# Optimization experiments

Measured on AMD Instinct MI355X. Metric: run time of the kernel, lower is better.

The kernel has to match this reference:

```python
import jax, jax.numpy as jnp
import numpy as np

D_MODEL = 1024
D_FF = 4096
EPS = 1e-6


def _rms_norm(x, eps=EPS):
    var = jnp.mean(x * x, axis=-1, keepdims=True) + eps
    return x * jax.lax.rsqrt(var)


def setup_inputs() -> dict:
    key = jax.random.key(0)
    kx, kw = jax.random.split(key)
    x = jax.random.normal(kx, (4, 4096, D_MODEL), dtype=jnp.float32)
    std = np.sqrt(2.0 / (D_FF + D_MODEL))
    # trunc_normal_(mean=0, std, a=-3std, b=3std) approximated by clipped normal
    w = jax.random.truncated_normal(kw, -3.0, 3.0, (D_FF, D_MODEL), dtype=jnp.float32) * std
    return {"x": x, "weight": w}


def reference(x, weight):
    # scores: [..., d_ff] = rmsnorm(x) @ rmsnorm(weight).T
    scores = jnp.einsum('bsd,cd->bsc', _rms_norm(x), _rms_norm(weight))
    probs = jax.nn.softmax(scores, axis=-1)
    return jnp.einsum('bsc,cd->bsd', probs, weight)
```

## Files before the change

kernel.cpp:

```cpp
#include <hip/hip_runtime.h>
#include <hip/hip_fp16.h>


#define D_MODEL 1024
#define D_FF    4096
#define M_ROWS  16384
#define MC      4096

typedef _Float16 half8 __attribute__((ext_vector_type(8)));
typedef _Float16 half4 __attribute__((ext_vector_type(4)));
typedef float    floatx4 __attribute__((ext_vector_type(4)));

__device__ __forceinline__ void gld_lds16(const void* g, void* l) {
  __builtin_amdgcn_global_load_lds(
      (const __attribute__((address_space(1))) void*)g,
      (__attribute__((address_space(3))) void*)l, 16, 0, 0);
}

#define MB_X (M_ROWS / 4)
#define MB_W (D_FF / 4)
__global__ __launch_bounds__(256) void rmsnorm_split_kernel(
    const float* __restrict__ X, _Float16* __restrict__ XH,
    _Float16* __restrict__ XL, const float* __restrict__ W,
    _Float16* __restrict__ WH, _Float16* __restrict__ WL) {
  const int lane = threadIdx.x & 63;
  const bool isW = blockIdx.x >= MB_X;
  const long row = (long)(isW ? blockIdx.x - MB_X : blockIdx.x) * 4 +
                   (threadIdx.x >> 6);
  const float* x = (isW ? W : X) + row * D_MODEL;
  _Float16* YH = (isW ? WH : XH) + row * D_MODEL;
  _Float16* YL = (isW ? WL : XL) + row * D_MODEL;

  float v[16];
  float ss = 0.f;
#pragma unroll
  for (int s = 0; s < 4; s++) {
    const float4 f = *(const float4*)(x + s * 256 + lane * 4);
    v[s * 4 + 0] = f.x; v[s * 4 + 1] = f.y;
    v[s * 4 + 2] = f.z; v[s * 4 + 3] = f.w;
    ss += f.x * f.x + f.y * f.y + f.z * f.z + f.w * f.w;
  }
#pragma unroll
  for (int off = 32; off >= 1; off >>= 1) ss += __shfl_xor(ss, off);
  const float inv = rsqrtf(ss * (1.0f / D_MODEL) + 1e-6f);
#pragma unroll
  for (int s = 0; s < 4; s++) {
    half4 h, l;
#pragma unroll
    for (int j = 0; j < 4; j++) {
      const float t = v[s * 4 + j] * inv;
      const _Float16 hi = (_Float16)t;
      h[j] = hi;
      l[j] = (_Float16)(t - (float)hi);
    }
    *(half4*)(YH + s * 256 + lane * 4) = h;
    *(half4*)(YL + s * 256 + lane * 4) = l;
  }
}

__global__ __launch_bounds__(256) void transpose_kernel(
    const float* __restrict__ W, _Float16* __restrict__ WT) {
  __shared__ _Float16 tile[32][33];
  const int tx = threadIdx.x & 31;
  const int ty = threadIdx.x >> 5;
  const int d0 = blockIdx.x * 32;
  const int c0 = blockIdx.y * 32;
#pragma unroll
  for (int i = 0; i < 32; i += 8)
    tile[ty + i][tx] = (_Float16)W[(long)(c0 + ty + i) * D_MODEL + d0 + tx];
  __syncthreads();
#pragma unroll
  for (int i = 0; i < 32; i += 8)
    WT[(long)(d0 + ty + i) * D_FF + c0 + tx] = tile[tx][ty + i];
}

__global__ __launch_bounds__(512, 2) void gemm1_kernel(
    const _Float16* __restrict__ XH, const _Float16* __restrict__ XL,
    const _Float16* __restrict__ WH, float* __restrict__ S) {
  __shared__ _Float16 Bs[2][256 * 64];
  __shared__ _Float16 Ah[2][128 * 64];
  __shared__ _Float16 Al[2][128 * 64];
  const int tid = threadIdx.x;
  const int lane = tid & 63;
  const int wave = tid >> 6;

  const int bid = blockIdx.y * 16 + blockIdx.x;
  const int swz = ((bid & 7) << 6) | (bid >> 3);
  const int bx = swz & 15, by = swz >> 4;
  const long rowBase = (long)by * 128;
  const long colBase = (long)bx * 256;

  const int srow = tid >> 3;
  const int scol = ((tid & 7) ^ (srow & 7)) * 8;
  const _Float16* Bg  = WH + (colBase + srow) * (long)D_MODEL + scol;
  const _Float16* Ahg = XH + (rowBase + srow) * (long)D_MODEL + scol;
  const _Float16* Alg = XL + (rowBase + srow) * (long)D_MODEL + scol;
  const int dstOff = tid * 8;

  const int wr = wave >> 2, wc = wave & 3;
  const int m16 = lane & 15, q = lane >> 4, mx7 = m16 & 7;
  const int aRow = wr * 64, bRow = wc * 64;

  floatx4 acc[4][4] = {};
  half8 b0[4], b1[4], a[4];

#define RD_A4(buf, ksl)                                                        \
  _Pragma("unroll") for (int mi = 0; mi < 4; mi++) a[mi] =                     \
      *(const half8*)(&buf[(aRow + mi * 16 + m16) * 64 +                       \
                           (((ksl)*4 + q) ^ mx7) * 8]);
#define RD_B4(buf, dst, ksl)                                                   \
  _Pragma("unroll") for (int ni = 0; ni < 4; ni++) dst[ni] =                   \
      *(const half8*)(&buf[(bRow + ni * 16 + m16) * 64 +                       \
                           (((ksl)*4 + q) ^ mx7) * 8]);
#define MFMA16(BF)                                                             \
  __builtin_amdgcn_s_setprio(1);                                               \
  _Pragma("unroll") for (int mi = 0; mi < 4; mi++)                             \
  _Pragma("unroll") for (int ni = 0; ni < 4; ni++)                             \
      acc[mi][ni] = __builtin_amdgcn_mfma_f32_16x16x32_f16(                    \
          a[mi], BF[ni], acc[mi][ni], 0, 0, 0);                                \
  __builtin_amdgcn_s_setprio(0);
#define BAR() __builtin_amdgcn_s_barrier()
#define LGKM0() asm volatile("s_waitcnt lgkmcnt(0)" ::: "memory")

  {
#pragma unroll
    for (int r = 0; r < 4; r++)
      gld_lds16(Bg + (long)r * 64 * D_MODEL, &Bs[0][r * 4096 + dstOff]);
#pragma unroll
    for (int r = 0; r < 2; r++)
      gld_lds16(Ahg + (long)r * 64 * D_MODEL, &Ah[0][r * 4096 + dstOff]);
#pragma unroll
    for (int r = 0; r < 2; r++)
      gld_lds16(Alg + (long)r * 64 * D_MODEL, &Al[0][r * 4096 + dstOff]);
    asm volatile("s_waitcnt vmcnt(2)" ::: "memory");
    BAR();
    __builtin_amdgcn_sched_barrier(0);
  }

  for (int i = 0; i < 16; i++) {
    const int cur = i & 1, nxt = cur ^ 1;
    const long ktn = (long)(i + 1) * 64;
    const bool lastI = (i == 15);

    RD_B4(Bs[cur], b0, 0);
    RD_A4(Ah[cur], 0);
    if (!lastI) {
      gld_lds16(Bg + (long)0 * 64 * D_MODEL + ktn, &Bs[nxt][0 * 4096 + dstOff]);
      gld_lds16(Bg + (long)1 * 64 * D_MODEL + ktn, &Bs[nxt][1 * 4096 + dstOff]);
    }
    BAR();
    LGKM0();
    MFMA16(b0);
    BAR();

    RD_B4(Bs[cur], b1, 1);
    RD_A4(Ah[cur], 1);
    if (!lastI) {
      gld_lds16(Bg + (long)2 * 64 * D_MODEL + ktn, &Bs[nxt][2 * 4096 + dstOff]);
      gld_lds16(Bg + (long)3 * 64 * D_MODEL + ktn, &Bs[nxt][3 * 4096 + dstOff]);
      asm volatile("s_waitcnt vmcnt(4)" ::: "memory");
    } else {
      asm volatile("s_waitcnt vmcnt(0)" ::: "memory");
    }
    BAR();
    LGKM0();
    MFMA16(b1);
    BAR();
    __builtin_amdgcn_sched_barrier(0);

    RD_A4(Al[cur], 0);
    if (!lastI) {
      gld_lds16(Ahg + (long)0 * 64 * D_MODEL + ktn, &Ah[nxt][0 * 4096 + dstOff]);
      gld_lds16(Ahg + (long)1 * 64 * D_MODEL + ktn, &Ah[nxt][1 * 4096 + dstOff]);
    }
    BAR();
    LGKM0();
    MFMA16(b0);
    BAR();

    RD_A4(Al[cur], 1);
    if (!lastI) {
      gld_lds16(Alg + (long)0 * 64 * D_MODEL + ktn, &Al[nxt][0 * 4096 + dstOff]);
      gld_lds16(Alg + (long)1 * 64 * D_MODEL + ktn, &Al[nxt][1 * 4096 + dstOff]);
      asm volatile("s_waitcnt vmcnt(2)" ::: "memory");
    }
    BAR();
    LGKM0();
    MFMA16(b1);
    BAR();
    __builtin_amdgcn_sched_barrier(0);
  }
#undef RD_A4
#undef RD_B4
#undef MFMA16
#undef BAR
#undef LGKM0

#pragma unroll
  for (int mi = 0; mi < 4; mi++)
#pragma unroll
    for (int r = 0; r < 4; r++) {
      const long rr = rowBase + wr * 64 + mi * 16 + q * 4 + r;
#pragma unroll
      for (int ni = 0; ni < 4; ni++)
        S[rr * D_FF + colBase + wc * 64 + ni * 16 + m16] = acc[mi][ni][r];
    }
}

__global__ __launch_bounds__(256, 2) void gemm2_kernel(
    const _Float16* __restrict__ P, const _Float16* __restrict__ WT,
    float* __restrict__ O) {
  constexpr int BK = 128, K = D_FF, LDA = 2 * D_FF, KSPLIT = 2048;
  __shared__ _Float16 As[128 * BK];
  __shared__ _Float16 Bs[128 * BK];
  const int tid = threadIdx.x;
  const int wave = tid >> 6, lane = tid & 63;

  const int bid = ((blockIdx.z * 32 + blockIdx.y) << 3) | blockIdx.x;
  const int swz = ((bid & 7) << 6) | (bid >> 3);
  const int bx = swz & 7;
  const int by = (swz >> 3) & 31;
  const int bz = swz >> 8;

  const long rowBase = (long)by * 128;
  const long colBase = (long)bx * 128;
  const int k0 = bz * KSPLIT;

  const int srow4 = lane >> 4;
  const int slotE = (lane & 15) ^ srow4;
  const int slotO = slotE ^ 4;
  const _Float16* AgE = P + (rowBase + wave * 32 + srow4) * (long)LDA + slotE * 8;
  const _Float16* AgO = P + (rowBase + wave * 32 + srow4) * (long)LDA + slotO * 8;
  const _Float16* BgE = WT + (colBase + wave * 32 + srow4) * (long)K + slotE * 8;
  const _Float16* BgO = WT + (colBase + wave * 32 + srow4) * (long)K + slotO * 8;
  _Float16* AsW = As + wave * 4096 + lane * 8;
  _Float16* BsW = Bs + wave * 4096 + lane * 8;
  const int wr = wave >> 1, wc = wave & 1;
  const int m16 = lane & 15, q = lane >> 4;
  const int mx7 = m16 & 7;

  floatx4 acc[4][4] = {};

  for (int kt = k0; kt < k0 + KSPLIT; kt += BK) {
#pragma unroll
    for (int i = 0; i < 8; i++) {
      const _Float16* ag = (i & 1) ? AgO : AgE;
      const _Float16* bg = (i & 1) ? BgO : BgE;
      gld_lds16(ag + (long)i * 4 * LDA + kt, AsW + i * 512);
      gld_lds16(bg + (long)i * 4 * K + kt, BsW + i * 512);
    }
    __syncthreads();
#pragma unroll
    for (int ks = 0; ks < 4; ks++) {
      const int kx = ((ks * 4 + q) ^ mx7) * 8;
      half8 a[4], b[4];
#pragma unroll
      for (int mi = 0; mi < 4; mi++)
        a[mi] = *(const half8*)(&As[(wr * 64 + mi * 16 + m16) * BK + kx]);
#pragma unroll
      for (int ni = 0; ni < 4; ni++)
        b[ni] = *(const half8*)(&Bs[(wc * 64 + ni * 16 + m16) * BK + kx]);
#pragma unroll
      for (int mi = 0; mi < 4; mi++)
#pragma unroll
        for (int ni = 0; ni < 4; ni++)
          acc[mi][ni] = __builtin_amdgcn_mfma_f32_16x16x32_f16(
              a[mi], b[ni], acc[mi][ni], 0, 0, 0);
    }
    __syncthreads();
  }

#pragma unroll
  for (int mi = 0; mi < 4; mi++)
#pragma unroll
    for (int r = 0; r < 4; r++) {
      const long rr = rowBase + wr * 64 + mi * 16 + q * 4 + r;
#pragma unroll
      for (int ni = 0; ni < 4; ni++)
        unsafeAtomicAdd(&O[rr * D_MODEL + colBase + wc * 64 + ni * 16 + m16],
                        acc[mi][ni][r]);
    }
}

__global__ __launch_bounds__(256) void softmax_kernel(float* __restrict__ S) {
  float* s = S + (long)blockIdx.x * D_FF;
  const int t = threadIdx.x;
  const int lane = t & 63, wave = t >> 6;
  __shared__ float redm[4], redl[4];

  float v[16];
  float mx = -3.4e38f;
#pragma unroll
  for (int seg = 0; seg < 4; seg++) {
    const float4 f = *(const float4*)(s + seg * 1024 + t * 4);
    v[seg * 4 + 0] = f.x; v[seg * 4 + 1] = f.y;
    v[seg * 4 + 2] = f.z; v[seg * 4 + 3] = f.w;
  }
#pragma unroll
  for (int j = 0; j < 16; j++) mx = fmaxf(mx, v[j]);
#pragma unroll
  for (int off = 32; off >= 1; off >>= 1) mx = fmaxf(mx, __shfl_xor(mx, off));
  if (lane == 0) redm[wave] = mx;
  __syncthreads();
  const float m = fmaxf(fmaxf(redm[0], redm[1]), fmaxf(redm[2], redm[3]));

  float sum = 0.f;
#pragma unroll
  for (int j = 0; j < 16; j++) {
    v[j] = __expf(v[j] - m);
    sum += v[j];
  }
#pragma unroll
  for (int off = 32; off >= 1; off >>= 1) sum += __shfl_xor(sum, off);
  if (lane == 0) redl[wave] = sum;
  __syncthreads();
  const float inv = 1.f / (redl[0] + redl[1] + redl[2] + redl[3]);

  _Float16* p = (_Float16*)s;
#pragma unroll
  for (int seg = 0; seg < 4; seg++) {
    half4 h;
#pragma unroll
    for (int j = 0; j < 4; j++) h[j] = (_Float16)(v[seg * 4 + j] * inv);
    *(half4*)(p + seg * 1024 + t * 4) = h;
  }
}

extern "C" void kernel_launch(void* const* d_in, const int* in_sizes, int n_in,
                              void* d_out, int out_size, void* d_ws, size_t ws_size,
                              hipStream_t stream) {
  const float* x = (const float*)d_in[0];
  const float* w = (const float*)d_in[1];
  float* out = (float*)d_out;

  const size_t NEED = 152ull << 20;
  if (ws_size < NEED) return;

  char* ws = (char*)d_ws;
  _Float16* xh = (_Float16*)(ws);
  _Float16* xl = (_Float16*)(ws + (32ull << 20));
  _Float16* wh = (_Float16*)(ws + (64ull << 20));
  _Float16* wl = (_Float16*)(ws + (72ull << 20));
  _Float16* wT = (_Float16*)(ws + (80ull << 20));
  float*    S  = (float*)   (ws + (88ull << 20));

  hipMemsetAsync(d_out, 0, (size_t)M_ROWS * D_MODEL * sizeof(float), stream);

  hipLaunchKernelGGL(rmsnorm_split_kernel, dim3(MB_X + MB_W), dim3(256), 0,
                     stream, x, xh, xl, w, wh, wl);
  hipLaunchKernelGGL(transpose_kernel, dim3(D_MODEL / 32, D_FF / 32), dim3(256),
                     0, stream, w, wT);

  for (int c = 0; c < M_ROWS / MC; c++) {
    const long ro = (long)c * MC;
    hipLaunchKernelGGL(gemm1_kernel, dim3(D_FF / 256, MC / 128), dim3(512), 0,
                       stream, xh + ro * D_MODEL, xl + ro * D_MODEL, wh, S);
    hipLaunchKernelGGL(softmax_kernel, dim3(MC), dim3(256), 0, stream, S);
    hipLaunchKernelGGL(gemm2_kernel, dim3(D_MODEL / 128, MC / 128, 2),
                       dim3(256), 0, stream, (const _Float16*)S, wT,
                       out + ro * D_MODEL);
  }
}
```

Before: 665.2 us.

## Enlarge gemm1 tile to 256x256 with single-buffered A halves and staged loads

Doubles the gemm1 block tile from 128x256 to 256x256 rows, so each wave accumulates 128x64 outputs. The B tile is reused across twice as many rows and the grid shrinks to 16x16. The hi and lo A tiles are now single-buffered and refilled while MFMAs run in quarter sub-steps, which keeps LDS within budget. This cuts global and LDS traffic per FLOP but raises register pressure (acc[8][4]) and adds more barriers and tighter load/compute ordering. With launch_bounds(512,2), the larger LDS footprint and register count may lower occupancy.

```diff
diff --git a/kernel.cpp b/kernel.cpp
--- a/kernel.cpp
+++ b/kernel.cpp
@@ -77,17 +77,16 @@
 __global__ __launch_bounds__(512, 2) void gemm1_kernel(
     const _Float16* __restrict__ XH, const _Float16* __restrict__ XL,
     const _Float16* __restrict__ WH, float* __restrict__ S) {
-  __shared__ _Float16 Bs[2][256 * 64];
-  __shared__ _Float16 Ah[2][128 * 64];
-  __shared__ _Float16 Al[2][128 * 64];
+  __shared__ _Float16 Bs2[2][256 * 64];
+  __shared__ _Float16 AhT[256 * 64];
+  __shared__ _Float16 AlT[256 * 64];
   const int tid = threadIdx.x;
-  const int lane = tid & 63;
-  const int wave = tid >> 6;
+  const int lane = tid & 63, wave = tid >> 6;
 
   const int bid = blockIdx.y * 16 + blockIdx.x;
-  const int swz = ((bid & 7) << 6) | (bid >> 3);
-  const int bx = swz & 15, by = swz >> 4;
-  const long rowBase = (long)by * 128;
+  const int lg = ((bid & 7) << 5) | (bid >> 3);
+  const int by = lg >> 4, bx = lg & 15;
+  const long rowBase = (long)by * 256;
   const long colBase = (long)bx * 256;
 
   const int srow = tid >> 3;
@@ -99,111 +98,106 @@
 
   const int wr = wave >> 2, wc = wave & 3;
   const int m16 = lane & 15, q = lane >> 4, mx7 = m16 & 7;
-  const int aRow = wr * 64, bRow = wc * 64;
-
-  floatx4 acc[4][4] = {};
-  half8 b0[4], b1[4], a[4];
-
-#define RD_A4(buf, ksl)                                                        \
-  _Pragma("unroll") for (int mi = 0; mi < 4; mi++) a[mi] =                     \
-      *(const half8*)(&buf[(aRow + mi * 16 + m16) * 64 +                       \
-                           (((ksl)*4 + q) ^ mx7) * 8]);
-#define RD_B4(buf, dst, ksl)                                                   \
-  _Pragma("unroll") for (int ni = 0; ni < 4; ni++) dst[ni] =                   \
-      *(const half8*)(&buf[(bRow + ni * 16 + m16) * 64 +                       \
-                           (((ksl)*4 + q) ^ mx7) * 8]);
-#define MFMA16(BF)                                                             \
+  const int aBase = wr * 128, bBase = wc * 64;
+
+  floatx4 acc[8][4] = {};
+  half8 a[2][4], b[2][4];
+
+#define LD_A(T, QR)                                                            \
+  _Pragma("unroll") for (int ks = 0; ks < 2; ks++)                             \
+  _Pragma("unroll") for (int mf = 0; mf < 4; mf++)                             \
+      a[ks][mf] = *(const half8*)(&T[(aBase + (QR)*64 + mf * 16 + m16) * 64 +  \
+                                     (((ks * 4 + q) ^ mx7)) * 8]);
+#define LD_B(CUR, QC)                                                          \
+  _Pragma("unroll") for (int ks = 0; ks < 2; ks++)                             \
+  _Pragma("unroll") for (int nf = 0; nf < 2; nf++)                             \
+      b[ks][(QC)*2 + nf] =                                                     \
+          *(const half8*)(&Bs2[CUR][(bBase + (QC)*32 + nf * 16 + m16) * 64 +   \
+                                    (((ks * 4 + q) ^ mx7)) * 8]);
+#define MM(QR, QC)                                                             \
   __builtin_amdgcn_s_setprio(1);                                               \
-  _Pragma("unroll") for (int mi = 0; mi < 4; mi++)                             \
-  _Pragma("unroll") for (int ni = 0; ni < 4; ni++)                             \
-      acc[mi][ni] = __builtin_amdgcn_mfma_f32_16x16x32_f16(                    \
-          a[mi], BF[ni], acc[mi][ni], 0, 0, 0);                                \
+  _Pragma("unroll") for (int ks = 0; ks < 2; ks++)                             \
+  _Pragma("unroll") for (int mf = 0; mf < 4; mf++)                             \
+  _Pragma("unroll") for (int nf = 0; nf < 2; nf++)                             \
+      acc[(QR)*4 + mf][(QC)*2 + nf] = __builtin_amdgcn_mfma_f32_16x16x32_f16(  \
+          a[ks][mf], b[ks][(QC)*2 + nf], acc[(QR)*4 + mf][(QC)*2 + nf],        \
+          0, 0, 0);                                                            \
   __builtin_amdgcn_s_setprio(0);
+#define STG(G, T, R, KT) \
+  gld_lds16((G) + (long)(R)*64 * D_MODEL + (KT), &(T)[(R)*4096 + dstOff]);
 #define BAR() __builtin_amdgcn_s_barrier()
-#define LGKM0() asm volatile("s_waitcnt lgkmcnt(0)" ::: "memory")
 
   {
 #pragma unroll
-    for (int r = 0; r < 4; r++)
-      gld_lds16(Bg + (long)r * 64 * D_MODEL, &Bs[0][r * 4096 + dstOff]);
-#pragma unroll
-    for (int r = 0; r < 2; r++)
-      gld_lds16(Ahg + (long)r * 64 * D_MODEL, &Ah[0][r * 4096 + dstOff]);
-#pragma unroll
-    for (int r = 0; r < 2; r++)
-      gld_lds16(Alg + (long)r * 64 * D_MODEL, &Al[0][r * 4096 + dstOff]);
-    asm volatile("s_waitcnt vmcnt(2)" ::: "memory");
+    for (int r = 0; r < 4; r++) STG(Bg, Bs2[0], r, 0);
+#pragma unroll
+    for (int r = 0; r < 4; r++) STG(Ahg, AhT, r, 0);
+    asm volatile("s_waitcnt vmcnt(0)" ::: "memory");
     BAR();
     __builtin_amdgcn_sched_barrier(0);
   }
 
+#pragma unroll 2
   for (int i = 0; i < 16; i++) {
     const int cur = i & 1, nxt = cur ^ 1;
-    const long ktn = (long)(i + 1) * 64;
-    const bool lastI = (i == 15);
-
-    RD_B4(Bs[cur], b0, 0);
-    RD_A4(Ah[cur], 0);
-    if (!lastI) {
-      gld_lds16(Bg + (long)0 * 64 * D_MODEL + ktn, &Bs[nxt][0 * 4096 + dstOff]);
-      gld_lds16(Bg + (long)1 * 64 * D_MODEL + ktn, &Bs[nxt][1 * 4096 + dstOff]);
-    }
-    BAR();
-    LGKM0();
-    MFMA16(b0);
-    BAR();
-
-    RD_B4(Bs[cur], b1, 1);
-    RD_A4(Ah[cur], 1);
-    if (!lastI) {
-      gld_lds16(Bg + (long)2 * 64 * D_MODEL + ktn, &Bs[nxt][2 * 4096 + dstOff]);
-      gld_lds16(Bg + (long)3 * 64 * D_MODEL + ktn, &Bs[nxt][3 * 4096 + dstOff]);
+    const long kt0 = (long)i * 64, kt1 = kt0 + 64;
+    const bool last = (i == 15);
+
+    LD_A(AhT, 0);
+    LD_B(cur, 0);
+    STG(Alg, AlT, 0, kt0);
+    STG(Alg, AlT, 1, kt0);
+    BAR(); MM(0, 0); BAR();
+
+    LD_B(cur, 1);
+    STG(Alg, AlT, 2, kt0);
+    STG(Alg, AlT, 3, kt0);
+    BAR(); MM(0, 1); BAR();
+
+    LD_A(AhT, 1);
+    if (!last) { STG(Bg, Bs2[nxt], 0, kt1); STG(Bg, Bs2[nxt], 1, kt1); }
+    BAR(); MM(1, 0); BAR();
+
+    if (!last) {
+      STG(Bg, Bs2[nxt], 2, kt1);
+      STG(Bg, Bs2[nxt], 3, kt1);
       asm volatile("s_waitcnt vmcnt(4)" ::: "memory");
     } else {
       asm volatile("s_waitcnt vmcnt(0)" ::: "memory");
     }
-    BAR();
-    LGKM0();
-    MFMA16(b1);
-    BAR();
+    BAR(); MM(1, 1); BAR();
     __builtin_amdgcn_sched_barrier(0);
 
-    RD_A4(Al[cur], 0);
-    if (!lastI) {
-      gld_lds16(Ahg + (long)0 * 64 * D_MODEL + ktn, &Ah[nxt][0 * 4096 + dstOff]);
-      gld_lds16(Ahg + (long)1 * 64 * D_MODEL + ktn, &Ah[nxt][1 * 4096 + dstOff]);
-    }
-    BAR();
-    LGKM0();
-    MFMA16(b0);
-    BAR();
-
-    RD_A4(Al[cur], 1);
-    if (!lastI) {
-      gld_lds16(Alg + (long)0 * 64 * D_MODEL + ktn, &Al[nxt][0 * 4096 + dstOff]);
-      gld_lds16(Alg + (long)1 * 64 * D_MODEL + ktn, &Al[nxt][1 * 4096 + dstOff]);
-      asm volatile("s_waitcnt vmcnt(2)" ::: "memory");
-    }
-    BAR();
-    LGKM0();
-    MFMA16(b1);
-    BAR();
+    LD_A(AlT, 0);
+    if (!last) { STG(Ahg, AhT, 0, kt1); STG(Ahg, AhT, 1, kt1); }
+    BAR(); MM(0, 0); BAR();
+
+    if (!last) { STG(Ahg, AhT, 2, kt1); STG(Ahg, AhT, 3, kt1); }
+    BAR(); MM(0, 1); BAR();
+
+    LD_A(AlT, 1);
+    BAR(); MM(1, 0); BAR();
+
+    if (!last) asm volatile("s_waitcnt vmcnt(0)" ::: "memory");
+    BAR(); MM(1, 1); BAR();
     __builtin_amdgcn_sched_barrier(0);
   }
-#undef RD_A4
-#undef RD_B4
-#undef MFMA16
+#undef LD_A
+#undef LD_B
+#undef MM
+#undef STG
 #undef BAR
-#undef LGKM0
-
-#pragma unroll
-  for (int mi = 0; mi < 4; mi++)
+
+#pragma unroll
+  for (int ai = 0; ai < 8; ai++)
 #pragma unroll
     for (int r = 0; r < 4; r++) {
-      const long rr = rowBase + wr * 64 + mi * 16 + q * 4 + r;
-#pragma unroll
-      for (int ni = 0; ni < 4; ni++)
-        S[rr * D_FF + colBase + wc * 64 + ni * 16 + m16] = acc[mi][ni][r];
+      const long rr =
+          rowBase + wr * 128 + (ai >> 2) * 64 + (ai & 3) * 16 + q * 4 + r;
+#pragma unroll
+      for (int bi = 0; bi < 4; bi++)
+        S[rr * D_FF + colBase + wc * 64 + (bi >> 1) * 32 + (bi & 1) * 16 +
+          m16] = acc[ai][bi][r];
     }
 }
 
@@ -353,7 +347,7 @@
 
   for (int c = 0; c < M_ROWS / MC; c++) {
     const long ro = (long)c * MC;
-    hipLaunchKernelGGL(gemm1_kernel, dim3(D_FF / 256, MC / 128), dim3(512), 0,
+    hipLaunchKernelGGL(gemm1_kernel, dim3(16, 16), dim3(512), 0,
                        stream, xh + ro * D_MODEL, xl + ro * D_MODEL, wh, S);
     hipLaunchKernelGGL(softmax_kernel, dim3(MC), dim3(256), 0, stream, S);
     hipLaunchKernelGGL(gemm2_kernel, dim3(D_MODEL / 128, MC / 128, 2),
```

After: 690.5 us. 3.8% more time.
